# Performance work log

Measured on AMD Instinct MI355X. Metric: run time of the kernel, lower is better.

## Reference

```python
import jax, jax.numpy as jnp
import numpy as np

B, T, VG, S = 64, 256, 1232, 32
LW, VW = 64, 8000
N_TAGS = 8
BLANK = 0
IGNORE_INDEX = 0
TAG_FACTOR = 0.1
GLOSS_W = 1.0
WORD_W = 1.0
NEG = -1e30


def setup_inputs() -> dict:
    key = jax.random.key(0)
    k1, k2, k3, k4, k5, k6 = jax.random.split(key, 6)
    glosses = jax.random.randint(k1, (B, S), 1, VG)            # CTC targets (avoid blank=0)
    words = jax.random.randint(k2, (B, LW), 0, VW)             # translation targets
    glosses_scores = jax.random.normal(k3, (B, T, VG), jnp.float32)
    words_output = jax.nn.log_softmax(jax.random.normal(k4, (B, LW, VW), jnp.float32), axis=-1)
    frames_len = jnp.full((B,), T, jnp.int32)
    glosses_len = jax.random.randint(k5, (B,), 1, S + 1).astype(jnp.int32)
    tag_ids = jax.random.randint(k6, (VG,), 0, N_TAGS).astype(jnp.int32)
    return {"glosses": glosses, "words": words, "glosses_scores": glosses_scores,
            "words_output": words_output, "frames_len": frames_len,
            "glosses_len": glosses_len, "tag_ids": tag_ids}


def booster_scores(scores, tag_ids):
    # per-tag mean over vocab dim, gathered back per vocab entry
    onehot = jax.nn.one_hot(tag_ids, N_TAGS, dtype=scores.dtype)   # [V, n_tags]
    counts = onehot.sum(axis=0)                                    # [n_tags]
    tag_mean = jnp.einsum('btv,vn->btn', scores, onehot) / counts  # [B,T,n_tags]
    return scores + TAG_FACTOR * tag_mean[..., tag_ids]            # [B,T,V]


def ctc_loss_sum(log_probs, targets, input_lens, target_lens):
    # log_probs [B,T,V], targets [B,S]
    Bb, Tt, _ = log_probs.shape
    Ss = targets.shape[1]
    L = 2 * Ss + 1
    ext = jnp.full((Bb, L), BLANK, dtype=targets.dtype).at[:, 1::2].set(targets)  # blank-interleaved
    lp_ext = jnp.take_along_axis(log_probs, jnp.broadcast_to(ext[:, None, :], (Bb, Tt, L)), axis=2)  # [B,T,L]
    prev2 = jnp.pad(ext, ((0, 0), (2, 0)), constant_values=BLANK)[:, :L]
    can_skip = (ext != BLANK) & (ext != prev2)                    # [B,L]

    alpha0 = jnp.full((Bb, L), NEG, log_probs.dtype)
    alpha0 = alpha0.at[:, 0].set(lp_ext[:, 0, 0]).at[:, 1].set(lp_ext[:, 0, 1])

    lp_t = jnp.swapaxes(lp_ext, 0, 1)  # [T,B,L]

    def step(alpha, xs):
        lp, t = xs
        a1 = jnp.concatenate([jnp.full((Bb, 1), NEG, alpha.dtype), alpha[:, :-1]], axis=1)
        a2 = jnp.concatenate([jnp.full((Bb, 2), NEG, alpha.dtype), alpha[:, :-2]], axis=1)
        a2 = jnp.where(can_skip, a2, NEG)
        m = jnp.maximum(alpha, jnp.maximum(a1, a2))
        new = m + jnp.log(jnp.exp(alpha - m) + jnp.exp(a1 - m) + jnp.exp(a2 - m)) + lp
        valid = (t < input_lens)[:, None]
        return jnp.where(valid, new, alpha), None

    alpha, _ = jax.lax.scan(step, alpha0, (lp_t[1:], jnp.arange(1, Tt)))

    idx1 = 2 * target_lens.astype(jnp.int32)
    idx0 = jnp.maximum(idx1 - 1, 0)
    aN = jnp.take_along_axis(alpha, jnp.stack([idx0, idx1], axis=1), axis=1)  # [B,2]
    loss = -jax.nn.logsumexp(aN, axis=1)
    loss = jnp.where(loss > 1e29, 0.0, loss)  # zero_infinity
    return loss.sum()


def nll_loss_sum(log_probs, targets):
    # input = words_output.permute(0,2,1)[:,:,:-1], target = words[:,1:]
    lp = log_probs[:, :-1, :]          # [B, LW-1, VW]
    tgt = targets[:, 1:]               # [B, LW-1]
    g = jnp.take_along_axis(lp, tgt[..., None], axis=2)[..., 0]
    mask = tgt != IGNORE_INDEX
    return -jnp.where(mask, g, 0.0).sum()


def reference(glosses, words, glosses_scores, words_output, frames_len, glosses_len, tag_ids):
    boosted = booster_scores(glosses_scores, tag_ids)          # training=True path
    glosses_probs = jax.nn.log_softmax(boosted, axis=-1)
    recognition_loss = ctc_loss_sum(glosses_probs, glosses, frames_len, glosses_len)
    translation_loss = nll_loss_sum(words_output, words)
    total = GLOSS_W * recognition_loss + WORD_W * translation_loss
    return (total, recognition_loss, translation_loss)
```

## Files before the change

kernel.cpp:

```cpp
#include <hip/hip_runtime.h>

#define B_    64
#define T_    256
#define VG_   1232
#define S_    32
#define LW_   64
#define VW_   8000
#define NTAGS 8
#define NEG_  (-1e30f)
#define LP_STRIDE 34
#define LOG2E 1.44269504088896340736f
#define LN2   0.69314718055994530942f

__device__ __forceinline__ float exp2g(float x) {
    float r; asm("v_exp_f32 %0, %1" : "=v"(r) : "v"(x)); return r;
}
__device__ __forceinline__ float log2g(float x) {
    float r; asm("v_log_f32 %0, %1" : "=v"(r) : "v"(x)); return r;
}
__device__ __forceinline__ void st_agent(float* p, float v) {
    __hip_atomic_store(p, v, __ATOMIC_RELAXED, __HIP_MEMORY_SCOPE_AGENT);
}
__device__ __forceinline__ float ld_agent(const float* p) {
    return __hip_atomic_load(p, __ATOMIC_RELAXED, __HIP_MEMORY_SCOPE_AGENT);
}
__device__ __forceinline__ float dpp_shr1(float x, float fill) {
    int r = __builtin_amdgcn_update_dpp(
        __builtin_bit_cast(int, fill), __builtin_bit_cast(int, x),
        0x138, 0xF, 0xF, false);
    return __builtin_bit_cast(float, r);
}
template <int CTRL>
__device__ __forceinline__ float dpp_add(float x) {
    int s = __builtin_amdgcn_update_dpp(
        0, __builtin_bit_cast(int, x), CTRL, 0xF, 0xF, true);
    return x + __builtin_bit_cast(float, s);
}
__device__ __forceinline__ float wave_sum_to0(float x) {
    x = dpp_add<0x101>(x);
    x = dpp_add<0x102>(x);
    x = dpp_add<0x104>(x);
    x = dpp_add<0x108>(x);
    x += __shfl_xor(x, 16, 64);
    x += __shfl_xor(x, 32, 64);
    return x;
}

__global__ __launch_bounds__(256) void kA_booster(
    const float* __restrict__ scores, const int* __restrict__ tag_ids,
    const int* __restrict__ glosses, float* __restrict__ lp_ws,
    int* __restrict__ counter)
{
    __shared__ float tm2L[4][NTAGS];
    const int tid  = threadIdx.x;
    const int lane = tid & 63;
    const int wv   = tid >> 6;
    const int row  = blockIdx.x * 4 + wv;
    const int b    = row >> 8;

    if (blockIdx.x == 0 && tid == 0) *counter = 0;

    const float* srow = scores + (size_t)row * VG_;

    const int gidx = (lane >= 1 && lane < 33) ? glosses[b * S_ + lane - 1] : 0;

    float4 sv[5];
    int4   tv[5];
#pragma unroll
    for (int i = 0; i < 5; ++i) {
        const int idx = i * 64 + lane;
        const bool act = (i < 4) || (lane < 52);
        sv[i] = act ? ((const float4*)srow)[idx]  : make_float4(0.f, 0.f, 0.f, 0.f);
        tv[i] = act ? ((const int4*)tag_ids)[idx] : make_int4(0, 0, 0, 0);
    }
    const float gval = srow[gidx];
    const int   gtag = tag_ids[gidx];

    float sums[NTAGS], cntf[NTAGS];
#pragma unroll
    for (int n = 0; n < NTAGS; ++n) { sums[n] = 0.f; cntf[n] = 0.f; }
#pragma unroll
    for (int i = 0; i < 5; ++i) {
        const float xs[4] = {sv[i].x, sv[i].y, sv[i].z, sv[i].w};
        const int   ts[4] = {tv[i].x, tv[i].y, tv[i].z, tv[i].w};
#pragma unroll
        for (int j = 0; j < 4; ++j) {
#pragma unroll
            for (int n = 0; n < NTAGS; ++n) {
                const bool eq = (ts[j] == n);
                sums[n] += eq ? xs[j] : 0.f;
                cntf[n] += eq ? 1.0f : 0.f;
            }
        }
    }
#pragma unroll
    for (int n = 0; n < NTAGS; ++n) {
        sums[n] = wave_sum_to0(sums[n]);
        cntf[n] = wave_sum_to0(cntf[n]);
    }

    if (lane == 0) {
        cntf[0] -= 48.0f;
#pragma unroll
        for (int n = 0; n < NTAGS; ++n)
            tm2L[wv][n] = (0.1f * LOG2E) * sums[n] *
                          __builtin_amdgcn_rcpf(cntf[n]);
    }
    __builtin_amdgcn_sched_barrier(0);

    float se = 0.f;
#pragma unroll
    for (int i = 0; i < 5; ++i) {
        const float xs[4] = {sv[i].x, sv[i].y, sv[i].z, sv[i].w};
        const int   ts[4] = {tv[i].x, tv[i].y, tv[i].z, tv[i].w};
        const bool act = (i < 4) || (lane < 52);
#pragma unroll
        for (int j = 0; j < 4; ++j) {
            const float e = exp2g(fmaf(xs[j], LOG2E, tm2L[wv][ts[j]]));
            se += act ? e : 0.f;
        }
    }
    se = wave_sum_to0(se);
    const float se0 = __builtin_bit_cast(
        float, __builtin_amdgcn_readfirstlane(__builtin_bit_cast(int, se)));
    const float lse2 = log2g(se0);

    if (lane < 33) {
        const float v = fmaf(gval, LOG2E, tm2L[wv][gtag]) - lse2;
        lp_ws[(size_t)row * LP_STRIDE + lane] = v;
    }
}

template <bool FULL>
__device__ __forceinline__ void scan_body(
    const float* __restrict__ tile, int lane, int off, bool ok2, int Tlen,
    float& alpha, float& a64)
{
    auto STEP = [&](int t, float lp, float lpB) {
        const float a1 = dpp_shr1(alpha, NEG_);
        float a2 = dpp_shr1(a1, NEG_);
        a2 = ok2 ? a2 : NEG_;
        const float m3 = fmaxf(alpha, fmaxf(a1, a2));
        const float e0 = exp2g(alpha - m3);
        const float e1 = exp2g(a1 - m3);
        const float e2 = exp2g(a2 - m3);
        const float nw = (m3 + lp) + log2g((e0 + e1) + e2);
        const float m2 = fmaxf(a64, alpha);
        const float n64 = (m2 + lpB) + log2g(exp2g(a64 - m2) + exp2g(alpha - m2));
        if (FULL || t < Tlen) { alpha = nw; a64 = n64; }
    };

    float cur[4], curB[4];
#pragma unroll
    for (int j = 0; j < 4; ++j) {
        cur[j]  = tile[(1 + j) * LP_STRIDE + off];
        curB[j] = tile[(1 + j) * LP_STRIDE];
    }
    int tbase = 1;
    for (int g = 0; g < 63; ++g) {
        float nxt[4], nxtB[4];
        const int tb2 = tbase + 4;
#pragma unroll
        for (int j = 0; j < 4; ++j) {
            nxt[j]  = tile[(tb2 + j) * LP_STRIDE + off];
            nxtB[j] = tile[(tb2 + j) * LP_STRIDE];
        }
#pragma unroll
        for (int j = 0; j < 4; ++j) STEP(tbase + j, cur[j], curB[j]);
#pragma unroll
        for (int j = 0; j < 4; ++j) { cur[j] = nxt[j]; curB[j] = nxtB[j]; }
        tbase += 4;
    }
#pragma unroll
    for (int j = 0; j < 3; ++j) STEP(253 + j, cur[j], curB[j]);
}

__global__ __launch_bounds__(256) void kB_ctc_nll_final(
    const float* __restrict__ lp_ws, const int* __restrict__ glosses,
    const int* __restrict__ frames_len, const int* __restrict__ glosses_len,
    const int* __restrict__ words, const float* __restrict__ words_out,
    float* __restrict__ loss_ws, float* __restrict__ nll_ws,
    int* __restrict__ counter, float* __restrict__ out)
{
    __shared__ __align__(16) float tile[(T_ + 1) * LP_STRIDE];
    const int tid = threadIdx.x;
    const int b   = blockIdx.x;

    float nacc = 0.f;
    if (tid < LW_ - 1) {
        const int tgt = words[b * LW_ + tid + 1];
        if (tgt != 0)
            nacc = -words_out[((size_t)b * LW_ + tid) * VW_ + tgt];
    }

    {
        const float4* src4 = (const float4*)(lp_ws + (size_t)b * T_ * LP_STRIDE);
        float4* dst4 = (float4*)tile;
        float4 r[9];
#pragma unroll
        for (int i = 0; i < 9; ++i) {
            const int idx = i * 256 + tid;
            if (idx < 2176) r[i] = src4[idx];
        }
#pragma unroll
        for (int i = 0; i < 9; ++i) {
            const int idx = i * 256 + tid;
            if (idx < 2176) dst4[idx] = r[i];
        }
    }
    __syncthreads();
    if (tid >= 64) return;
    const int lane = tid;

    const bool odd  = (lane & 1) != 0;
    const int  sIdx = (lane - 1) >> 1;
    bool ok2 = false;
    if (odd && sIdx >= 1) {
        const int g  = glosses[b * S_ + sIdx];
        const int gp = glosses[b * S_ + sIdx - 1];
        ok2 = (g != gp) && (g != 0);
    }
    const int off = odd ? (1 + sIdx) : 0;

    float alpha = NEG_;
    float a64   = NEG_;
    {
        const float lp00 = tile[off];
        if (lane <= 1) alpha = lp00;
    }
    const int Tlen = frames_len[b];

    if (Tlen == T_) scan_body<true >(tile, lane, off, ok2, Tlen, alpha, a64);
    else            scan_body<false>(tile, lane, off, ok2, Tlen, alpha, a64);

    const float a64v = __shfl(a64, 63, 64);
    const int i1 = 2 * glosses_len[b];
    const int i0 = i1 - 1;
    const float A0 = __shfl(alpha, i0, 64);
    const float A1 = (i1 >= 64) ? a64v : __shfl(alpha, i1, 64);
    const float mm = fmaxf(A0, A1);
    float loss = -(mm + log2g(exp2g(A0 - mm) + exp2g(A1 - mm))) * LN2;
    if (loss > 1e29f) loss = 0.f;

    nacc = wave_sum_to0(nacc);
    if (lane == 0) {
        st_agent(&loss_ws[b], loss);
        st_agent(&nll_ws[b], nacc);
    }

    asm volatile("s_waitcnt vmcnt(0)" ::: "memory");
    int old = 0;
    if (lane == 0) old = atomicAdd(counter, 1);
    old = __shfl(old, 0, 64);
    if (old == B_ - 1) {
        float v = ld_agent(&loss_ws[lane]);
        float u = ld_agent(&nll_ws[lane]);
#pragma unroll
        for (int o = 32; o >= 1; o >>= 1) {
            v += __shfl_xor(v, o, 64);
            u += __shfl_xor(u, o, 64);
        }
        if (lane == 0) {
            out[0] = v + u;
            out[1] = v;
            out[2] = u;
        }
    }
}

extern "C" void kernel_launch(void* const* d_in, const int* in_sizes, int n_in,
                              void* d_out, int out_size, void* d_ws, size_t ws_size,
                              hipStream_t stream) {
    const int*   glosses     = (const int*)d_in[0];
    const int*   words       = (const int*)d_in[1];
    const float* scores      = (const float*)d_in[2];
    const float* words_out   = (const float*)d_in[3];
    const int*   frames_len  = (const int*)d_in[4];
    const int*   glosses_len = (const int*)d_in[5];
    const int*   tag_ids     = (const int*)d_in[6];
    float* out = (float*)d_out;

    float* w       = (float*)d_ws;
    int*   counter = (int*)d_ws;
    float* loss_ws = w + 16;
    float* nll_ws  = w + 96;
    float* lp_ws   = w + 192;

    kA_booster<<<(B_ * T_) / 4, 256, 0, stream>>>(scores, tag_ids, glosses,
                                                  lp_ws, counter);
    kB_ctc_nll_final<<<B_, 256, 0, stream>>>(lp_ws, glosses, frames_len,
                                             glosses_len, words, words_out,
                                             loss_ws, nll_ws, counter, out);
}
```

Measured before the change: 52.70 us.

## Store CTC log-probs as fp16 and interleave two batch scans per wave

The booster kernel now writes the gathered log-probs in half precision, which halves the workspace traffic. The CTC kernel now runs one 64-thread wave per block and processes two batch items in an interleaved recurrence, so independent exp/log chains can hide each other's latency. Because the recurrence is latency-bound, interleaving two chains should improve ILP, at the cost of half as many blocks (32). Half precision adds rounding error to the log-probabilities, which may affect loss accuracy.

```diff
diff --git a/kernel.cpp b/kernel.cpp
--- a/kernel.cpp
+++ b/kernel.cpp
@@ -1,4 +1,5 @@
 #include <hip/hip_runtime.h>
+#include <hip/hip_fp16.h>
 
 #define B_    64
 #define T_    256
@@ -9,6 +10,7 @@
 #define NTAGS 8
 #define NEG_  (-1e30f)
 #define LP_STRIDE 34
+#define TILE_H 8768
 #define LOG2E 1.44269504088896340736f
 #define LN2   0.69314718055994530942f
 
@@ -48,7 +50,7 @@
 
 __global__ __launch_bounds__(256) void kA_booster(
     const float* __restrict__ scores, const int* __restrict__ tag_ids,
-    const int* __restrict__ glosses, float* __restrict__ lp_ws,
+    const int* __restrict__ glosses, __half* __restrict__ lp_h,
     int* __restrict__ counter)
 {
     __shared__ float tm2L[4][NTAGS];
@@ -127,132 +129,155 @@
 
     if (lane < 33) {
         const float v = fmaf(gval, LOG2E, tm2L[wv][gtag]) - lse2;
-        lp_ws[(size_t)row * LP_STRIDE + lane] = v;
-    }
-}
-
-template <bool FULL>
-__device__ __forceinline__ void scan_body(
-    const float* __restrict__ tile, int lane, int off, bool ok2, int Tlen,
-    float& alpha, float& a64)
-{
-    auto STEP = [&](int t, float lp, float lpB) {
-        const float a1 = dpp_shr1(alpha, NEG_);
-        float a2 = dpp_shr1(a1, NEG_);
-        a2 = ok2 ? a2 : NEG_;
-        const float m3 = fmaxf(alpha, fmaxf(a1, a2));
-        const float e0 = exp2g(alpha - m3);
-        const float e1 = exp2g(a1 - m3);
-        const float e2 = exp2g(a2 - m3);
-        const float nw = (m3 + lp) + log2g((e0 + e1) + e2);
-        const float m2 = fmaxf(a64, alpha);
-        const float n64 = (m2 + lpB) + log2g(exp2g(a64 - m2) + exp2g(alpha - m2));
-        if (FULL || t < Tlen) { alpha = nw; a64 = n64; }
-    };
-
-    float cur[4], curB[4];
-#pragma unroll
-    for (int j = 0; j < 4; ++j) {
-        cur[j]  = tile[(1 + j) * LP_STRIDE + off];
-        curB[j] = tile[(1 + j) * LP_STRIDE];
-    }
-    int tbase = 1;
-    for (int g = 0; g < 63; ++g) {
-        float nxt[4], nxtB[4];
-        const int tb2 = tbase + 4;
-#pragma unroll
-        for (int j = 0; j < 4; ++j) {
-            nxt[j]  = tile[(tb2 + j) * LP_STRIDE + off];
-            nxtB[j] = tile[(tb2 + j) * LP_STRIDE];
-        }
-#pragma unroll
-        for (int j = 0; j < 4; ++j) STEP(tbase + j, cur[j], curB[j]);
-#pragma unroll
-        for (int j = 0; j < 4; ++j) { cur[j] = nxt[j]; curB[j] = nxtB[j]; }
-        tbase += 4;
-    }
-#pragma unroll
-    for (int j = 0; j < 3; ++j) STEP(253 + j, cur[j], curB[j]);
-}
-
-__global__ __launch_bounds__(256) void kB_ctc_nll_final(
-    const float* __restrict__ lp_ws, const int* __restrict__ glosses,
+        lp_h[(size_t)row * LP_STRIDE + lane] = __float2half(v);
+    }
+}
+
+__global__ __launch_bounds__(64) void kB_ctc_nll_final(
+    const __half* __restrict__ lp_h, const int* __restrict__ glosses,
     const int* __restrict__ frames_len, const int* __restrict__ glosses_len,
     const int* __restrict__ words, const float* __restrict__ words_out,
     float* __restrict__ loss_ws, float* __restrict__ nll_ws,
     int* __restrict__ counter, float* __restrict__ out)
 {
-    __shared__ __align__(16) float tile[(T_ + 1) * LP_STRIDE];
-    const int tid = threadIdx.x;
-    const int b   = blockIdx.x;
-
-    float nacc = 0.f;
-    if (tid < LW_ - 1) {
-        const int tgt = words[b * LW_ + tid + 1];
-        if (tgt != 0)
-            nacc = -words_out[((size_t)b * LW_ + tid) * VW_ + tgt];
+    __shared__ __align__(16) unsigned short tiles[2][TILE_H];
+    const int lane = threadIdx.x;
+    const int blk  = blockIdx.x;
+    const int b0 = blk * 2, b1 = blk * 2 + 1;
+
+    float nacc0 = 0.f, nacc1 = 0.f;
+    if (lane < LW_ - 1) {
+        const int t0 = words[b0 * LW_ + lane + 1];
+        const int t1 = words[b1 * LW_ + lane + 1];
+        if (t0 != 0) nacc0 = -words_out[((size_t)b0 * LW_ + lane) * VW_ + t0];
+        if (t1 != 0) nacc1 = -words_out[((size_t)b1 * LW_ + lane) * VW_ + t1];
     }
 
     {
-        const float4* src4 = (const float4*)(lp_ws + (size_t)b * T_ * LP_STRIDE);
-        float4* dst4 = (float4*)tile;
-        float4 r[9];
-#pragma unroll
-        for (int i = 0; i < 9; ++i) {
-            const int idx = i * 256 + tid;
-            if (idx < 2176) r[i] = src4[idx];
-        }
-#pragma unroll
-        for (int i = 0; i < 9; ++i) {
-            const int idx = i * 256 + tid;
-            if (idx < 2176) dst4[idx] = r[i];
-        }
+        const float4* s0 = (const float4*)(lp_h + (size_t)b0 * T_ * LP_STRIDE);
+        const float4* s1 = (const float4*)(lp_h + (size_t)b1 * T_ * LP_STRIDE);
+        float4* d0 = (float4*)tiles[0];
+        float4* d1 = (float4*)tiles[1];
+        float4 r[17];
+#pragma unroll
+        for (int i = 0; i < 17; ++i) r[i] = s0[i * 64 + lane];
+#pragma unroll
+        for (int i = 0; i < 17; ++i) d0[i * 64 + lane] = r[i];
+#pragma unroll
+        for (int i = 0; i < 17; ++i) r[i] = s1[i * 64 + lane];
+#pragma unroll
+        for (int i = 0; i < 17; ++i) d1[i * 64 + lane] = r[i];
     }
     __syncthreads();
-    if (tid >= 64) return;
-    const int lane = tid;
+
+    const __half* t0h = (const __half*)tiles[0];
+    const __half* t1h = (const __half*)tiles[1];
 
     const bool odd  = (lane & 1) != 0;
     const int  sIdx = (lane - 1) >> 1;
-    bool ok2 = false;
+    bool ok2_0 = false, ok2_1 = false;
     if (odd && sIdx >= 1) {
-        const int g  = glosses[b * S_ + sIdx];
-        const int gp = glosses[b * S_ + sIdx - 1];
-        ok2 = (g != gp) && (g != 0);
+        const int g0  = glosses[b0 * S_ + sIdx];
+        const int gp0 = glosses[b0 * S_ + sIdx - 1];
+        ok2_0 = (g0 != gp0) && (g0 != 0);
+        const int g1  = glosses[b1 * S_ + sIdx];
+        const int gp1 = glosses[b1 * S_ + sIdx - 1];
+        ok2_1 = (g1 != gp1) && (g1 != 0);
     }
     const int off = odd ? (1 + sIdx) : 0;
 
-    float alpha = NEG_;
-    float a64   = NEG_;
-    {
-        const float lp00 = tile[off];
-        if (lane <= 1) alpha = lp00;
-    }
-    const int Tlen = frames_len[b];
-
-    if (Tlen == T_) scan_body<true >(tile, lane, off, ok2, Tlen, alpha, a64);
-    else            scan_body<false>(tile, lane, off, ok2, Tlen, alpha, a64);
-
-    const float a64v = __shfl(a64, 63, 64);
-    const int i1 = 2 * glosses_len[b];
-    const int i0 = i1 - 1;
-    const float A0 = __shfl(alpha, i0, 64);
-    const float A1 = (i1 >= 64) ? a64v : __shfl(alpha, i1, 64);
-    const float mm = fmaxf(A0, A1);
-    float loss = -(mm + log2g(exp2g(A0 - mm) + exp2g(A1 - mm))) * LN2;
-    if (loss > 1e29f) loss = 0.f;
-
-    nacc = wave_sum_to0(nacc);
+    float al0 = NEG_, a64_0 = NEG_;
+    float al1 = NEG_, a64_1 = NEG_;
+    if (lane <= 1) {
+        al0 = __half2float(t0h[off]);
+        al1 = __half2float(t1h[off]);
+    }
+    const int Tlen0 = frames_len[b0];
+    const int Tlen1 = frames_len[b1];
+
+    auto STEP2 = [&](int t, float lp0, float lpB0, float lp1, float lpB1) {
+        const float a1_0 = dpp_shr1(al0, NEG_);
+        const float a1_1 = dpp_shr1(al1, NEG_);
+        float a2_0 = dpp_shr1(a1_0, NEG_);
+        float a2_1 = dpp_shr1(a1_1, NEG_);
+        a2_0 = ok2_0 ? a2_0 : NEG_;
+        a2_1 = ok2_1 ? a2_1 : NEG_;
+        const float m3_0 = fmaxf(al0, fmaxf(a1_0, a2_0));
+        const float m3_1 = fmaxf(al1, fmaxf(a1_1, a2_1));
+        const float s3_0 = (exp2g(al0 - m3_0) + exp2g(a1_0 - m3_0)) + exp2g(a2_0 - m3_0);
+        const float s3_1 = (exp2g(al1 - m3_1) + exp2g(a1_1 - m3_1)) + exp2g(a2_1 - m3_1);
+        const float nw0 = (m3_0 + lp0) + log2g(s3_0);
+        const float nw1 = (m3_1 + lp1) + log2g(s3_1);
+        const float m2_0 = fmaxf(a64_0, al0);
+        const float m2_1 = fmaxf(a64_1, al1);
+        const float n64_0 = (m2_0 + lpB0) + log2g(exp2g(a64_0 - m2_0) + exp2g(al0 - m2_0));
+        const float n64_1 = (m2_1 + lpB1) + log2g(exp2g(a64_1 - m2_1) + exp2g(al1 - m2_1));
+        if (t < Tlen0) { al0 = nw0; a64_0 = n64_0; }
+        if (t < Tlen1) { al1 = nw1; a64_1 = n64_1; }
+    };
+
+    float c0[4], cB0[4], c1[4], cB1[4];
+#pragma unroll
+    for (int j = 0; j < 4; ++j) {
+        c0[j]  = __half2float(t0h[(1 + j) * LP_STRIDE + off]);
+        cB0[j] = __half2float(t0h[(1 + j) * LP_STRIDE]);
+        c1[j]  = __half2float(t1h[(1 + j) * LP_STRIDE + off]);
+        cB1[j] = __half2float(t1h[(1 + j) * LP_STRIDE]);
+    }
+    int tbase = 1;
+    for (int g = 0; g < 63; ++g) {
+        float n0[4], nB0[4], n1[4], nB1[4];
+        const int tb2 = tbase + 4;
+#pragma unroll
+        for (int j = 0; j < 4; ++j) {
+            n0[j]  = __half2float(t0h[(tb2 + j) * LP_STRIDE + off]);
+            nB0[j] = __half2float(t0h[(tb2 + j) * LP_STRIDE]);
+            n1[j]  = __half2float(t1h[(tb2 + j) * LP_STRIDE + off]);
+            nB1[j] = __half2float(t1h[(tb2 + j) * LP_STRIDE]);
+        }
+#pragma unroll
+        for (int j = 0; j < 4; ++j)
+            STEP2(tbase + j, c0[j], cB0[j], c1[j], cB1[j]);
+#pragma unroll
+        for (int j = 0; j < 4; ++j) {
+            c0[j] = n0[j]; cB0[j] = nB0[j];
+            c1[j] = n1[j]; cB1[j] = nB1[j];
+        }
+        tbase += 4;
+    }
+#pragma unroll
+    for (int j = 0; j < 3; ++j)
+        STEP2(253 + j, c0[j], cB0[j], c1[j], cB1[j]);
+
+    const float a64v0 = __shfl(a64_0, 63, 64);
+    const float a64v1 = __shfl(a64_1, 63, 64);
+    const int i1_0 = 2 * glosses_len[b0];
+    const int i1_1 = 2 * glosses_len[b1];
+    const float A0_0 = __shfl(al0, i1_0 - 1, 64);
+    const float A1_0 = (i1_0 >= 64) ? a64v0 : __shfl(al0, i1_0, 64);
+    const float A0_1 = __shfl(al1, i1_1 - 1, 64);
+    const float A1_1 = (i1_1 >= 64) ? a64v1 : __shfl(al1, i1_1, 64);
+    const float mm0 = fmaxf(A0_0, A1_0);
+    const float mm1 = fmaxf(A0_1, A1_1);
+    float loss0 = -(mm0 + log2g(exp2g(A0_0 - mm0) + exp2g(A1_0 - mm0))) * LN2;
+    float loss1 = -(mm1 + log2g(exp2g(A0_1 - mm1) + exp2g(A1_1 - mm1))) * LN2;
+    if (loss0 > 1e29f) loss0 = 0.f;
+    if (loss1 > 1e29f) loss1 = 0.f;
+
+    nacc0 = wave_sum_to0(nacc0);
+    nacc1 = wave_sum_to0(nacc1);
     if (lane == 0) {
-        st_agent(&loss_ws[b], loss);
-        st_agent(&nll_ws[b], nacc);
+        st_agent(&loss_ws[b0], loss0);
+        st_agent(&loss_ws[b1], loss1);
+        st_agent(&nll_ws[b0], nacc0);
+        st_agent(&nll_ws[b1], nacc1);
     }
 
     asm volatile("s_waitcnt vmcnt(0)" ::: "memory");
     int old = 0;
     if (lane == 0) old = atomicAdd(counter, 1);
     old = __shfl(old, 0, 64);
-    if (old == B_ - 1) {
+    if (old == 31) {
         float v = ld_agent(&loss_ws[lane]);
         float u = ld_agent(&nll_ws[lane]);
 #pragma unroll
@@ -280,15 +305,15 @@
     const int*   tag_ids     = (const int*)d_in[6];
     float* out = (float*)d_out;
 
-    float* w       = (float*)d_ws;
-    int*   counter = (int*)d_ws;
-    float* loss_ws = w + 16;
-    float* nll_ws  = w + 96;
-    float* lp_ws   = w + 192;
+    float*  w       = (float*)d_ws;
+    int*    counter = (int*)d_ws;
+    float*  loss_ws = w + 16;
+    float*  nll_ws  = w + 96;
+    __half* lp_h    = (__half*)(w + 192);
 
     kA_booster<<<(B_ * T_) / 4, 256, 0, stream>>>(scores, tag_ids, glosses,
-                                                  lp_ws, counter);
-    kB_ctc_nll_final<<<B_, 256, 0, stream>>>(lp_ws, glosses, frames_len,
-                                             glosses_len, words, words_out,
-                                             loss_ws, nll_ws, counter, out);
-}
+                                                  lp_h, counter);
+    kB_ctc_nll_final<<<B_ / 2, 64, 0, stream>>>(lp_h, glosses, frames_len,
+                                                glosses_len, words, words_out,
+                                                loss_ws, nll_ws, counter, out);
+}
```

Result: slower. 74.56 us (median of 2 runs) (+41.5%).
